# Kernel optimization log

Measured on AMD Instinct MI355X. Metric: run time of the kernel, lower is better.

Reference implementation:

```python
import jax, jax.numpy as jnp
import numpy as np

TOP_K = 2
NUM_MOE_LAYERS = 4


def _gemma_mlp(x, w_gate, w_up, w_down):
    # x: [B,S,H]; w_gate/w_up: [H,I]; w_down: [I,H]
    h = jax.nn.gelu(x @ w_gate, approximate=True) * (x @ w_up)
    return h @ w_down


def setup_inputs() -> dict:
    key = jax.random.key(0)
    ks = jax.random.split(key, 8)
    B, S, H, I = 64, 512, 1024, 4096
    E_skill, E_shared = 8, 1
    sd_h = 1.0 / np.sqrt(H)
    sd_i = 1.0 / np.sqrt(I)
    return {
        "x": jax.random.normal(ks[0], (B, S, H), dtype=jnp.float32),
        "router_logits": jax.random.normal(ks[1], (B, E_skill), dtype=jnp.float32),
        "skill_gate": jax.random.normal(ks[2], (E_skill, H, I), dtype=jnp.float32) * sd_h,
        "skill_up": jax.random.normal(ks[3], (E_skill, H, I), dtype=jnp.float32) * sd_h,
        "skill_down": jax.random.normal(ks[4], (E_skill, I, H), dtype=jnp.float32) * sd_i,
        "shared_gate": jax.random.normal(ks[5], (E_shared, H, I), dtype=jnp.float32) * sd_h,
        "shared_up": jax.random.normal(ks[6], (E_shared, H, I), dtype=jnp.float32) * sd_h,
        "shared_down": jax.random.normal(ks[7], (E_shared, I, H), dtype=jnp.float32) * sd_i,
    }


def reference(x, router_logits, skill_gate, skill_up, skill_down,
              shared_gate, shared_up, shared_down):
    E = skill_gate.shape[0]
    # --- router: softmax in fp32, top-k, renormalize ---
    rw = jax.nn.softmax(router_logits.astype(jnp.float32), axis=-1)  # [B,E]
    topw, sel = jax.lax.top_k(rw, TOP_K)                              # [B,k]
    topw = topw / jnp.sum(topw, axis=-1, keepdims=True)
    topw = topw.astype(x.dtype)
    # ScaleGradient: identity fwd, grad scaled by 1/num_moe_layers
    s = 1.0 / NUM_MOE_LAYERS
    topw = topw * s + jax.lax.stop_gradient(topw * (1.0 - s))
    # combine weight per (sequence, expert): zero where expert not selected
    onehot = jax.nn.one_hot(sel, E, dtype=topw.dtype)                 # [B,k,E]
    w = jnp.einsum('bk,bke->be', topw, onehot)                        # [B,E]
    # --- skill experts: masked dense compute + weighted combine ---
    out = jnp.zeros_like(x)
    for e in range(E):
        y = _gemma_mlp(x, skill_gate[e], skill_up[e], skill_down[e])  # [B,S,H]
        out = out + w[:, e, None, None] * y
    # --- shared experts: dense, unweighted sum ---
    for j in range(shared_gate.shape[0]):
        out = out + _gemma_mlp(x, shared_gate[j], shared_up[j], shared_down[j])
    return out
```

## Files before the change

### kernel.cpp

```cpp
#include <hip/hip_runtime.h>
#include <hip/hip_fp16.h>

#define BB 64
#define SS 512
#define HH 1024
#define II 4096
#define EE 8

typedef _Float16 h8 __attribute__((ext_vector_type(8)));
typedef _Float16 h4 __attribute__((ext_vector_type(4)));
typedef float f4 __attribute__((ext_vector_type(4)));

typedef const __attribute__((address_space(1))) void* gas_t;
typedef __attribute__((address_space(3))) void* las_t;

__device__ __forceinline__ void gl_lds16(const void* g, void* l) {
  __builtin_amdgcn_global_load_lds((gas_t)g, (las_t)l, 16, 0, 0);
}

__device__ __forceinline__ int swzE(int row, int kslot) {
  return row * 32 + (((kslot ^ (row >> 1)) & 3) << 3);
}

__global__ void router_kernel(const float* __restrict__ logits,
                              int* __restrict__ sel, float* __restrict__ wsel) {
  int b = threadIdx.x;
  if (b >= BB) return;
  float l[EE];
  float mx = -1e30f;
  for (int e = 0; e < EE; ++e) { l[e] = logits[b * EE + e]; mx = fmaxf(mx, l[e]); }
  for (int e = 0; e < EE; ++e) l[e] = __expf(l[e] - mx);
  int i0 = 0;
  for (int e = 1; e < EE; ++e) if (l[e] > l[i0]) i0 = e;
  int i1 = (i0 == 0) ? 1 : 0;
  for (int e = 0; e < EE; ++e) if (e != i0 && l[e] > l[i1]) i1 = e;
  float t = l[i0] + l[i1];
  sel[b * 2 + 0] = i0; sel[b * 2 + 1] = i1;
  wsel[b * 2 + 0] = l[i0] / t; wsel[b * 2 + 1] = l[i1] / t;
}

__global__ void __launch_bounds__(256) cvt_x_kernel(const float* __restrict__ src,
                                                    _Float16* __restrict__ dst) {
  int i = blockIdx.x * 256 + threadIdx.x;
  const float4* s4 = (const float4*)src;
  float4 a = s4[2 * i], b = s4[2 * i + 1];
  h8 o = {(_Float16)a.x, (_Float16)a.y, (_Float16)a.z, (_Float16)a.w,
          (_Float16)b.x, (_Float16)b.y, (_Float16)b.z, (_Float16)b.w};
  *((h8*)dst + i) = o;
}

__global__ void __launch_bounds__(256) tcvt_kernel(const float* __restrict__ src,
                                                   _Float16* __restrict__ dst,
                                                   int R, int C) {
  __shared__ float tile[32][33];
  size_t msz = (size_t)R * C;
  src += (size_t)blockIdx.z * msz;
  dst += (size_t)blockIdx.z * msz;
  int c0 = blockIdx.x * 32, r0 = blockIdx.y * 32;
  int t = threadIdx.x;
  int ir = t >> 3, ic = (t & 7) * 4;
  float4 v = *(const float4*)(src + (size_t)(r0 + ir) * C + c0 + ic);
  tile[ir][ic + 0] = v.x; tile[ir][ic + 1] = v.y;
  tile[ir][ic + 2] = v.z; tile[ir][ic + 3] = v.w;
  __syncthreads();
  h4 o;
  o[0] = (_Float16)tile[ic + 0][ir];
  o[1] = (_Float16)tile[ic + 1][ir];
  o[2] = (_Float16)tile[ic + 2][ir];
  o[3] = (_Float16)tile[ic + 3][ir];
  *(h4*)(dst + (size_t)(c0 + ir) * R + r0 + ic) = o;
}

__global__ void __launch_bounds__(256, 2)
moe_up_kernel(const _Float16* __restrict__ xf,
              const _Float16* __restrict__ sgT, const _Float16* __restrict__ suT,
              const _Float16* __restrict__ shgT, const _Float16* __restrict__ shuT,
              const int* __restrict__ sel, const float* __restrict__ wsel,
              _Float16* __restrict__ hbuf, int b0) {
  __shared__ _Float16 As[128 * 32];
  __shared__ _Float16 Bg[128 * 32];
  __shared__ _Float16 Bu[128 * 32];

  const int task = blockIdx.z;
  const int cb = task / 3, slot = task - cb * 3;
  const int b = b0 + cb;
  const _Float16 *Wg, *Wu;
  float wgt;
  if (slot < 2) {
    int e = sel[b * 2 + slot];
    wgt = wsel[b * 2 + slot];
    Wg = sgT + (size_t)e * II * HH;
    Wu = suT + (size_t)e * II * HH;
  } else {
    wgt = 1.0f; Wg = shgT; Wu = shuT;
  }
  const _Float16* A = xf + (size_t)b * SS * HH;
  const int m0 = blockIdx.x * 128, n0 = blockIdx.y * 128;
  const int tid = threadIdx.x, lane = tid & 63, wv = tid >> 6;
  const int wm = (wv >> 1) * 64, wn = (wv & 1) * 64;

  const int sr = tid >> 2;
  const int ksl = (tid & 3) ^ ((tid >> 3) & 3);
  const _Float16* ga0 = A + (size_t)(m0 + sr) * HH + ksl * 8;
  const _Float16* ga1 = A + (size_t)(m0 + 64 + sr) * HH + ksl * 8;
  const _Float16* gg0 = Wg + (size_t)(n0 + sr) * HH + ksl * 8;
  const _Float16* gg1 = Wg + (size_t)(n0 + 64 + sr) * HH + ksl * 8;
  const _Float16* gu0 = Wu + (size_t)(n0 + sr) * HH + ksl * 8;
  const _Float16* gu1 = Wu + (size_t)(n0 + 64 + sr) * HH + ksl * 8;

  const int ra = lane & 15, kq = lane >> 4;
  f4 accG[4][4] = {};
  f4 accU[4][4] = {};

  for (int k0 = 0; k0 < HH; k0 += 32) {
    gl_lds16(ga0 + k0, &As[wv * 512]);
    gl_lds16(ga1 + k0, &As[2048 + wv * 512]);
    gl_lds16(gg0 + k0, &Bg[wv * 512]);
    gl_lds16(gg1 + k0, &Bg[2048 + wv * 512]);
    gl_lds16(gu0 + k0, &Bu[wv * 512]);
    gl_lds16(gu1 + k0, &Bu[2048 + wv * 512]);
    __syncthreads();
    h8 af[4], bgf[4], buf_[4];
#pragma unroll
    for (int m = 0; m < 4; ++m) af[m] = *(const h8*)&As[swzE(wm + m * 16 + ra, kq)];
#pragma unroll
    for (int n = 0; n < 4; ++n) {
      bgf[n] = *(const h8*)&Bg[swzE(wn + n * 16 + ra, kq)];
      buf_[n] = *(const h8*)&Bu[swzE(wn + n * 16 + ra, kq)];
    }
#pragma unroll
    for (int m = 0; m < 4; ++m)
#pragma unroll
      for (int n = 0; n < 4; ++n) {
        accG[m][n] = __builtin_amdgcn_mfma_f32_16x16x32_f16(af[m], bgf[n], accG[m][n], 0, 0, 0);
        accU[m][n] = __builtin_amdgcn_mfma_f32_16x16x32_f16(af[m], buf_[n], accU[m][n], 0, 0, 0);
      }
    __syncthreads();
  }

  _Float16* hb = hbuf + (size_t)task * SS * II;
  const int rr = wm + (lane >> 4) * 4;
  const int cc = n0 + wn + ra;
#pragma unroll
  for (int m = 0; m < 4; ++m)
#pragma unroll
    for (int n = 0; n < 4; ++n)
#pragma unroll
      for (int r = 0; r < 4; ++r) {
        float g = accG[m][n][r];
        float u = accU[m][n][r];
        float z = 0.7978845608028654f * (g + 0.044715f * g * g * g);
        float ge = 0.5f * g * (1.0f + tanhf(z));
        int row = m0 + rr + m * 16 + r;
        int col = cc + n * 16;
        hb[(size_t)row * II + col] = (_Float16)(wgt * ge * u);
      }
}

__global__ void __launch_bounds__(256)
moe_down_kernel(const _Float16* __restrict__ hbuf,
                const _Float16* __restrict__ sdT, const _Float16* __restrict__ shdT,
                const int* __restrict__ sel,
                float* __restrict__ out, int b0) {
  __shared__ _Float16 As[128 * 32];
  __shared__ _Float16 Bs[128 * 32];

  const int cb = blockIdx.z, b = b0 + cb;
  const int m0 = blockIdx.x * 128, n0 = blockIdx.y * 128;
  const int tid = threadIdx.x, lane = tid & 63, wv = tid >> 6;
  const int wm = (wv >> 1) * 64, wn = (wv & 1) * 64;
  const int sr = tid >> 2;
  const int ksl = (tid & 3) ^ ((tid >> 3) & 3);
  const int ra = lane & 15, kq = lane >> 4;

  f4 acc[4][4] = {};

  for (int slot = 0; slot < 3; ++slot) {
    const _Float16* Ab = hbuf + (size_t)(cb * 3 + slot) * SS * II;
    const _Float16* Bt = (slot < 2) ? (sdT + (size_t)sel[b * 2 + slot] * HH * II) : shdT;
    const _Float16* ga0 = Ab + (size_t)(m0 + sr) * II + ksl * 8;
    const _Float16* ga1 = Ab + (size_t)(m0 + 64 + sr) * II + ksl * 8;
    const _Float16* gb0 = Bt + (size_t)(n0 + sr) * II + ksl * 8;
    const _Float16* gb1 = Bt + (size_t)(n0 + 64 + sr) * II + ksl * 8;
    for (int k0 = 0; k0 < II; k0 += 32) {
      gl_lds16(ga0 + k0, &As[wv * 512]);
      gl_lds16(ga1 + k0, &As[2048 + wv * 512]);
      gl_lds16(gb0 + k0, &Bs[wv * 512]);
      gl_lds16(gb1 + k0, &Bs[2048 + wv * 512]);
      __syncthreads();
      h8 af[4], bf[4];
#pragma unroll
      for (int m = 0; m < 4; ++m) af[m] = *(const h8*)&As[swzE(wm + m * 16 + ra, kq)];
#pragma unroll
      for (int n = 0; n < 4; ++n) bf[n] = *(const h8*)&Bs[swzE(wn + n * 16 + ra, kq)];
#pragma unroll
      for (int m = 0; m < 4; ++m)
#pragma unroll
        for (int n = 0; n < 4; ++n)
          acc[m][n] = __builtin_amdgcn_mfma_f32_16x16x32_f16(af[m], bf[n], acc[m][n], 0, 0, 0);
      __syncthreads();
    }
  }

  float* ob = out + (size_t)b * SS * HH;
  const int rr = wm + (lane >> 4) * 4;
  const int cc = n0 + wn + ra;
#pragma unroll
  for (int m = 0; m < 4; ++m)
#pragma unroll
    for (int n = 0; n < 4; ++n)
#pragma unroll
      for (int r = 0; r < 4; ++r)
        ob[(size_t)(m0 + rr + m * 16 + r) * HH + cc + n * 16] = acc[m][n][r];
}

extern "C" void kernel_launch(void* const* d_in, const int* in_sizes, int n_in,
                              void* d_out, int out_size, void* d_ws, size_t ws_size,
                              hipStream_t stream) {
  (void)in_sizes; (void)n_in; (void)out_size;
  const float* x = (const float*)d_in[0];
  const float* router_logits = (const float*)d_in[1];
  const float* skill_gate = (const float*)d_in[2];
  const float* skill_up = (const float*)d_in[3];
  const float* skill_down = (const float*)d_in[4];
  const float* shared_gate = (const float*)d_in[5];
  const float* shared_up = (const float*)d_in[6];
  const float* shared_down = (const float*)d_in[7];
  float* out = (float*)d_out;

  char* ws = (char*)d_ws;
  size_t off = 0;
  auto alloc = [&](size_t bytes) -> void* {
    void* p = ws + off;
    off += (bytes + 255) & ~(size_t)255;
    return p;
  };
  _Float16* xf  = (_Float16*)alloc((size_t)BB * SS * HH * 2);
  _Float16* sgT = (_Float16*)alloc((size_t)EE * II * HH * 2);
  _Float16* suT = (_Float16*)alloc((size_t)EE * II * HH * 2);
  _Float16* sdT = (_Float16*)alloc((size_t)EE * HH * II * 2);
  _Float16* shgT = (_Float16*)alloc((size_t)II * HH * 2);
  _Float16* shuT = (_Float16*)alloc((size_t)II * HH * 2);
  _Float16* shdT = (_Float16*)alloc((size_t)HH * II * 2);
  int* sel = (int*)alloc(BB * 2 * sizeof(int));
  float* wsel = (float*)alloc(BB * 2 * sizeof(float));

  const size_t hbytes1 = (size_t)3 * SS * II * 2;
  int chunk = 64;
  while (chunk > 1 && off + (size_t)chunk * hbytes1 > ws_size) chunk >>= 1;
  if (off + (size_t)chunk * hbytes1 > ws_size) return;
  _Float16* hbuf = (_Float16*)(ws + off);

  router_kernel<<<1, 64, 0, stream>>>(router_logits, sel, wsel);
  cvt_x_kernel<<<(BB * SS * HH) / 8 / 256, 256, 0, stream>>>(x, xf);
  tcvt_kernel<<<dim3(II / 32, HH / 32, EE), 256, 0, stream>>>(skill_gate, sgT, HH, II);
  tcvt_kernel<<<dim3(II / 32, HH / 32, EE), 256, 0, stream>>>(skill_up, suT, HH, II);
  tcvt_kernel<<<dim3(HH / 32, II / 32, EE), 256, 0, stream>>>(skill_down, sdT, II, HH);
  tcvt_kernel<<<dim3(II / 32, HH / 32, 1), 256, 0, stream>>>(shared_gate, shgT, HH, II);
  tcvt_kernel<<<dim3(II / 32, HH / 32, 1), 256, 0, stream>>>(shared_up, shuT, HH, II);
  tcvt_kernel<<<dim3(HH / 32, II / 32, 1), 256, 0, stream>>>(shared_down, shdT, II, HH);

  for (int b0 = 0; b0 < BB; b0 += chunk) {
    moe_up_kernel<<<dim3(SS / 128, II / 128, chunk * 3), 256, 0, stream>>>(
        xf, sgT, suT, shgT, shuT, sel, wsel, hbuf, b0);
    moe_down_kernel<<<dim3(SS / 128, HH / 128, chunk), 256, 0, stream>>>(
        hbuf, sdT, shdT, sel, out, b0);
  }
}
```

Baseline: 4.118 ms.

## Double-buffer LDS in MoE GEMMs, add XCD-aware block swizzle and fast GELU

Both the up and down MoE GEMM kernels now use two LDS buffers, so the next K-tile is loaded asynchronously while MFMAs run on the current one. This removes one barrier per iteration and hides load latency. Block indices are remapped so consecutive tiles sharing weights land on the same XCD for better L2 reuse. The tanh GELU is rewritten as a sigmoid form using exp and rcp. The up kernel drops its min-2-blocks launch bound, and the doubled LDS may reduce occupancy.

```diff
diff --git a/kernel.cpp b/kernel.cpp
--- a/kernel.cpp
+++ b/kernel.cpp
@@ -20,6 +20,15 @@
 
 __device__ __forceinline__ int swzE(int row, int kslot) {
   return row * 32 + (((kslot ^ (row >> 1)) & 3) << 3);
+}
+
+__device__ __forceinline__ int xcd_swz(int orig, int nwg) {
+  return (orig & 7) * (nwg >> 3) + (orig >> 3);
+}
+
+__device__ __forceinline__ float fast_gelu(float g) {
+  float t = 1.5957691216057308f * (g + 0.044715f * g * g * g);
+  return g * __builtin_amdgcn_rcpf(1.0f + __expf(-t));
 }
 
 __global__ void router_kernel(const float* __restrict__ logits,
@@ -71,17 +80,21 @@
   *(h4*)(dst + (size_t)(c0 + ir) * R + r0 + ic) = o;
 }
 
-__global__ void __launch_bounds__(256, 2)
+__global__ void __launch_bounds__(256)
 moe_up_kernel(const _Float16* __restrict__ xf,
               const _Float16* __restrict__ sgT, const _Float16* __restrict__ suT,
               const _Float16* __restrict__ shgT, const _Float16* __restrict__ shuT,
               const int* __restrict__ sel, const float* __restrict__ wsel,
               _Float16* __restrict__ hbuf, int b0) {
-  __shared__ _Float16 As[128 * 32];
-  __shared__ _Float16 Bg[128 * 32];
-  __shared__ _Float16 Bu[128 * 32];
-
-  const int task = blockIdx.z;
+  __shared__ _Float16 As[2][128 * 32];
+  __shared__ _Float16 Bg[2][128 * 32];
+  __shared__ _Float16 Bu[2][128 * 32];
+
+  const int nz = gridDim.z;
+  int orig = blockIdx.x + 4 * (blockIdx.y + 32 * blockIdx.z);
+  int swz = xcd_swz(orig, 128 * nz);
+  const int bm = swz & 3, bn = (swz >> 2) & 31, task = swz >> 7;
+
   const int cb = task / 3, slot = task - cb * 3;
   const int b = b0 + cb;
   const _Float16 *Wg, *Wu;
@@ -95,7 +108,7 @@
     wgt = 1.0f; Wg = shgT; Wu = shuT;
   }
   const _Float16* A = xf + (size_t)b * SS * HH;
-  const int m0 = blockIdx.x * 128, n0 = blockIdx.y * 128;
+  const int m0 = bm * 128, n0 = bn * 128;
   const int tid = threadIdx.x, lane = tid & 63, wv = tid >> 6;
   const int wm = (wv >> 1) * 64, wn = (wv & 1) * 64;
 
@@ -112,21 +125,22 @@
   f4 accG[4][4] = {};
   f4 accU[4][4] = {};
 
-  for (int k0 = 0; k0 < HH; k0 += 32) {
-    gl_lds16(ga0 + k0, &As[wv * 512]);
-    gl_lds16(ga1 + k0, &As[2048 + wv * 512]);
-    gl_lds16(gg0 + k0, &Bg[wv * 512]);
-    gl_lds16(gg1 + k0, &Bg[2048 + wv * 512]);
-    gl_lds16(gu0 + k0, &Bu[wv * 512]);
-    gl_lds16(gu1 + k0, &Bu[2048 + wv * 512]);
-    __syncthreads();
+  auto stage = [&](int bb, int k0) {
+    gl_lds16(ga0 + k0, &As[bb][wv * 512]);
+    gl_lds16(ga1 + k0, &As[bb][2048 + wv * 512]);
+    gl_lds16(gg0 + k0, &Bg[bb][wv * 512]);
+    gl_lds16(gg1 + k0, &Bg[bb][2048 + wv * 512]);
+    gl_lds16(gu0 + k0, &Bu[bb][wv * 512]);
+    gl_lds16(gu1 + k0, &Bu[bb][2048 + wv * 512]);
+  };
+  auto compute = [&](int bb) {
     h8 af[4], bgf[4], buf_[4];
 #pragma unroll
-    for (int m = 0; m < 4; ++m) af[m] = *(const h8*)&As[swzE(wm + m * 16 + ra, kq)];
+    for (int m = 0; m < 4; ++m) af[m] = *(const h8*)&As[bb][swzE(wm + m * 16 + ra, kq)];
 #pragma unroll
     for (int n = 0; n < 4; ++n) {
-      bgf[n] = *(const h8*)&Bg[swzE(wn + n * 16 + ra, kq)];
-      buf_[n] = *(const h8*)&Bu[swzE(wn + n * 16 + ra, kq)];
+      bgf[n] = *(const h8*)&Bg[bb][swzE(wn + n * 16 + ra, kq)];
+      buf_[n] = *(const h8*)&Bu[bb][swzE(wn + n * 16 + ra, kq)];
     }
 #pragma unroll
     for (int m = 0; m < 4; ++m)
@@ -135,8 +149,18 @@
         accG[m][n] = __builtin_amdgcn_mfma_f32_16x16x32_f16(af[m], bgf[n], accG[m][n], 0, 0, 0);
         accU[m][n] = __builtin_amdgcn_mfma_f32_16x16x32_f16(af[m], buf_[n], accU[m][n], 0, 0, 0);
       }
+  };
+
+  stage(0, 0);
+  __syncthreads();
+  int cur = 0;
+  for (int k0 = 32; k0 < HH; k0 += 32) {
+    stage(cur ^ 1, k0);
+    compute(cur);
     __syncthreads();
+    cur ^= 1;
   }
+  compute(cur);
 
   _Float16* hb = hbuf + (size_t)task * SS * II;
   const int rr = wm + (lane >> 4) * 4;
@@ -149,11 +173,9 @@
       for (int r = 0; r < 4; ++r) {
         float g = accG[m][n][r];
         float u = accU[m][n][r];
-        float z = 0.7978845608028654f * (g + 0.044715f * g * g * g);
-        float ge = 0.5f * g * (1.0f + tanhf(z));
         int row = m0 + rr + m * 16 + r;
         int col = cc + n * 16;
-        hb[(size_t)row * II + col] = (_Float16)(wgt * ge * u);
+        hb[(size_t)row * II + col] = (_Float16)(wgt * fast_gelu(g) * u);
       }
 }
 
@@ -162,44 +184,63 @@
                 const _Float16* __restrict__ sdT, const _Float16* __restrict__ shdT,
                 const int* __restrict__ sel,
                 float* __restrict__ out, int b0) {
-  __shared__ _Float16 As[128 * 32];
-  __shared__ _Float16 Bs[128 * 32];
-
-  const int cb = blockIdx.z, b = b0 + cb;
-  const int m0 = blockIdx.x * 128, n0 = blockIdx.y * 128;
+  __shared__ _Float16 As[2][128 * 32];
+  __shared__ _Float16 Bs[2][128 * 32];
+
+  const int nz = gridDim.z;
+  int orig = blockIdx.x + 4 * (blockIdx.y + 8 * blockIdx.z);
+  int swz = xcd_swz(orig, 32 * nz);
+  const int bm = swz & 3, bn = (swz >> 2) & 7, cb = swz >> 5;
+  const int b = b0 + cb;
+
+  const int m0 = bm * 128, n0 = bn * 128;
   const int tid = threadIdx.x, lane = tid & 63, wv = tid >> 6;
   const int wm = (wv >> 1) * 64, wn = (wv & 1) * 64;
   const int sr = tid >> 2;
   const int ksl = (tid & 3) ^ ((tid >> 3) & 3);
   const int ra = lane & 15, kq = lane >> 4;
 
+  const size_t slotStride = (size_t)SS * II;
+  const _Float16* a0 = hbuf + (size_t)(cb * 3) * slotStride + (size_t)(m0 + sr) * II + ksl * 8;
+  const size_t bof = (size_t)(n0 + sr) * II + ksl * 8;
+  const _Float16* pb0 = sdT + (size_t)sel[b * 2 + 0] * HH * II + bof;
+  const _Float16* pb1 = sdT + (size_t)sel[b * 2 + 1] * HH * II + bof;
+  const _Float16* pb2 = shdT + bof;
+
   f4 acc[4][4] = {};
 
-  for (int slot = 0; slot < 3; ++slot) {
-    const _Float16* Ab = hbuf + (size_t)(cb * 3 + slot) * SS * II;
-    const _Float16* Bt = (slot < 2) ? (sdT + (size_t)sel[b * 2 + slot] * HH * II) : shdT;
-    const _Float16* ga0 = Ab + (size_t)(m0 + sr) * II + ksl * 8;
-    const _Float16* ga1 = Ab + (size_t)(m0 + 64 + sr) * II + ksl * 8;
-    const _Float16* gb0 = Bt + (size_t)(n0 + sr) * II + ksl * 8;
-    const _Float16* gb1 = Bt + (size_t)(n0 + 64 + sr) * II + ksl * 8;
-    for (int k0 = 0; k0 < II; k0 += 32) {
-      gl_lds16(ga0 + k0, &As[wv * 512]);
-      gl_lds16(ga1 + k0, &As[2048 + wv * 512]);
-      gl_lds16(gb0 + k0, &Bs[wv * 512]);
-      gl_lds16(gb1 + k0, &Bs[2048 + wv * 512]);
-      __syncthreads();
-      h8 af[4], bf[4];
-#pragma unroll
-      for (int m = 0; m < 4; ++m) af[m] = *(const h8*)&As[swzE(wm + m * 16 + ra, kq)];
-#pragma unroll
-      for (int n = 0; n < 4; ++n) bf[n] = *(const h8*)&Bs[swzE(wn + n * 16 + ra, kq)];
-#pragma unroll
-      for (int m = 0; m < 4; ++m)
-#pragma unroll
-        for (int n = 0; n < 4; ++n)
-          acc[m][n] = __builtin_amdgcn_mfma_f32_16x16x32_f16(af[m], bf[n], acc[m][n], 0, 0, 0);
-      __syncthreads();
-    }
+  auto stage = [&](int bb, int t) {
+    int slot = t >> 7;
+    int k0 = (t & 127) << 5;
+    const _Float16* A0 = a0 + (size_t)slot * slotStride + k0;
+    const _Float16* Bp = (slot == 0 ? pb0 : (slot == 1 ? pb1 : pb2)) + k0;
+    gl_lds16(A0, &As[bb][wv * 512]);
+    gl_lds16(A0 + (size_t)64 * II, &As[bb][2048 + wv * 512]);
+    gl_lds16(Bp, &Bs[bb][wv * 512]);
+    gl_lds16(Bp + (size_t)64 * II, &Bs[bb][2048 + wv * 512]);
+  };
+  auto compute = [&](int bb) {
+    h8 af[4], bf[4];
+#pragma unroll
+    for (int m = 0; m < 4; ++m) af[m] = *(const h8*)&As[bb][swzE(wm + m * 16 + ra, kq)];
+#pragma unroll
+    for (int n = 0; n < 4; ++n) bf[n] = *(const h8*)&Bs[bb][swzE(wn + n * 16 + ra, kq)];
+#pragma unroll
+    for (int m = 0; m < 4; ++m)
+#pragma unroll
+      for (int n = 0; n < 4; ++n)
+        acc[m][n] = __builtin_amdgcn_mfma_f32_16x16x32_f16(af[m], bf[n], acc[m][n], 0, 0, 0);
+  };
+
+  const int TSTEPS = 3 * (II / 32);
+  stage(0, 0);
+  __syncthreads();
+  int cur = 0;
+  for (int t = 0; t < TSTEPS; ++t) {
+    if (t + 1 < TSTEPS) stage(cur ^ 1, t + 1);
+    compute(cur);
+    __syncthreads();
+    cur ^= 1;
   }
 
   float* ob = out + (size_t)b * SS * HH;
```

Measured after the change: 5.148 ms. +25.0%, slower.
